# Performance work log

Measured on AMD Instinct MI355X. Metric: run time of the kernel, lower is better.

The kernel has to match this reference:

```python
import jax, jax.numpy as jnp
import numpy as np

N, E = 10000, 320000
D, H, C = 256, 8, 32   # dim, heads, head_dim (dim//num_head)
DE, DF = 64, 1024      # edge_dim, dim_ff


def setup_inputs() -> dict:
    key = jax.random.key(0)
    ks = jax.random.split(key, 32)
    s = 0.05
    n = lambda k, shp: jax.random.normal(k, shp, jnp.float32) * s
    inp = {
        "nf": jax.random.normal(ks[0], (N, D), jnp.float32),
        "ei": jax.random.randint(ks[1], (2, E), 0, N),
        "ew": jax.random.normal(ks[2], (E, DE), jnp.float32),
        # GATConv 1
        "lin1": n(ks[3], (D, H * C)), "le1": n(ks[4], (DE, H * C)),
        "asrc1": n(ks[5], (H, C)), "adst1": n(ks[6], (H, C)), "aedge1": n(ks[7], (H, C)),
        "b1": jnp.zeros((H * C,), jnp.float32),
        # GATConv 2
        "lin2": n(ks[8], (D, H * C)), "le2": n(ks[9], (DE, H * C)),
        "asrc2": n(ks[10], (H, C)), "adst2": n(ks[11], (H, C)), "aedge2": n(ks[12], (H, C)),
        "b2": jnp.zeros((H * C,), jnp.float32),
        # LayerNorms
        "g1": jnp.ones((D,), jnp.float32), "be1": jnp.zeros((D,), jnp.float32),
        "g2": jnp.ones((D,), jnp.float32), "be2": jnp.zeros((D,), jnp.float32),
        "g3": jnp.ones((D,), jnp.float32), "be3": jnp.zeros((D,), jnp.float32),
        # FFN
        "w1": n(ks[13], (D, DF)), "fb1": jnp.zeros((DF,), jnp.float32),
        "w2": n(ks[14], (DF, D)), "fb2": jnp.zeros((D,), jnp.float32),
    }
    return inp


def _ln(x, g, b, eps=1e-6):
    # annotated-transformer LayerNorm: unbiased std, eps added to std
    mu = x.mean(-1, keepdims=True)
    sd = jnp.std(x, axis=-1, ddof=1, keepdims=True)
    return g * (x - mu) / (sd + eps) + b


def _gat(x, src, dst, ea, W, We, a_s, a_d, a_e, bias):
    # PyG GATConv with edge_dim, add_self_loops=True, fill_value='mean', concat=True
    ones = jnp.ones((src.shape[0], 1), x.dtype)
    cnt = jax.ops.segment_sum(ones, dst, num_segments=N)
    loop_attr = jax.ops.segment_sum(ea, dst, num_segments=N) / jnp.maximum(cnt, 1.0)
    idx = jnp.arange(N)
    srcf = jnp.concatenate([src, idx])
    dstf = jnp.concatenate([dst, idx])
    eaf = jnp.concatenate([ea, loop_attr], axis=0)          # [E+N, DE]
    xs = (x @ W).reshape(N, H, C)                            # [N,H,C]
    ef = (eaf @ We).reshape(-1, H, C)                        # [E+N,H,C]
    a_src = (xs * a_s).sum(-1)                               # [N,H]
    a_dst = (xs * a_d).sum(-1)                               # [N,H]
    alpha = a_src[srcf] + a_dst[dstf] + (ef * a_e).sum(-1)   # [E+N,H]
    alpha = jax.nn.leaky_relu(alpha, 0.2)
    m = jax.ops.segment_max(alpha, dstf, num_segments=N)     # segment softmax
    ex = jnp.exp(alpha - m[dstf])
    den = jax.ops.segment_sum(ex, dstf, num_segments=N)
    w = ex / (den[dstf] + 1e-16)                             # [E+N,H]
    out = jax.ops.segment_sum(w[:, :, None] * xs[srcf], dstf, num_segments=N)
    return out.reshape(N, H * C) + bias


def reference(nf, ei, ew, lin1, le1, asrc1, adst1, aedge1, b1,
              lin2, le2, asrc2, adst2, aedge2, b2,
              g1, be1, g2, be2, g3, be3, w1, fb1, w2, fb2):
    src, dst = ei[0], ei[1]
    h = _gat(nf, src, dst, ew, lin1, le1, asrc1, adst1, aedge1, b1)
    nf = nf + jax.nn.leaky_relu(_ln(h, g1, be1), 0.01)
    h = _gat(nf, src, dst, ew, lin2, le2, asrc2, adst2, aedge2, b2)
    nf = nf + jax.nn.leaky_relu(_ln(h, g2, be2), 0.01)
    h = jax.nn.relu(nf @ w1 + fb1) @ w2 + fb2
    nf = nf + jax.nn.leaky_relu(_ln(h, g3, be3), 0.01)
    return nf
```

## Files before the change

kernel.cpp:

```cpp
#include <hip/hip_runtime.h>
#include <hip/hip_bf16.h>
#include <math.h>

#define D 256
#define H 8
#define C 32
#define DE 64
#define DF 1024

static inline size_t align_up(size_t x, size_t a) { return (x + a - 1) / a * a; }

typedef __attribute__((ext_vector_type(8))) short short8;
typedef __attribute__((ext_vector_type(4))) float f32x4;

__device__ inline unsigned short f2b(float x) {
    __hip_bfloat16 h = __float2bfloat16(x);
    return *reinterpret_cast<unsigned short*>(&h);
}
__device__ inline float b2f(unsigned short u) {
    return __uint_as_float(((unsigned int)u) << 16);
}

__global__ void deg_kernel(const int* __restrict__ dst, int* __restrict__ deg, int E) {
    int e = blockIdx.x * 256 + threadIdx.x;
    if (e < E) atomicAdd(&deg[dst[e]], 1);
}

__global__ void partial_sum_kernel(const int* __restrict__ deg, int* __restrict__ part, int n) {
    int i = blockIdx.x * 256 + threadIdx.x;
    int v = (i < n) ? deg[i] : 0;
    for (int o = 1; o < 64; o <<= 1) v += __shfl_xor(v, o);
    __shared__ int w4[4];
    if ((threadIdx.x & 63) == 0) w4[threadIdx.x >> 6] = v;
    __syncthreads();
    if (threadIdx.x == 0) part[blockIdx.x] = w4[0] + w4[1] + w4[2] + w4[3];
}

__global__ void scan_part_kernel(int* __restrict__ part, int nb) {
    __shared__ int buf[256];
    int t = threadIdx.x;
    buf[t] = (t < nb) ? part[t] : 0;
    __syncthreads();
    for (int s = 1; s < 256; s <<= 1) {
        int v = (t >= s) ? buf[t - s] : 0;
        __syncthreads();
        buf[t] += v;
        __syncthreads();
    }
    int excl = (t == 0) ? 0 : buf[t - 1];
    if (t < nb) part[t] = excl;
}

__global__ void scan_final_kernel(const int* __restrict__ deg, const int* __restrict__ part,
                                  int* __restrict__ off, int* __restrict__ cursor, int n) {
    int b = blockIdx.x, t = threadIdx.x, i = b * 256 + t;
    __shared__ int buf[256];
    int v = (i < n) ? deg[i] : 0;
    buf[t] = v;
    __syncthreads();
    for (int s = 1; s < 256; s <<= 1) {
        int x = (t >= s) ? buf[t - s] : 0;
        __syncthreads();
        buf[t] += x;
        __syncthreads();
    }
    int excl = part[b] + buf[t] - v;
    if (i < n) { off[i] = excl; cursor[i] = excl; }
    if (i == n - 1) off[n] = excl + v;
}

__global__ void fill_kernel(const int* __restrict__ src, const int* __restrict__ dst,
                            int* __restrict__ cursor, int* __restrict__ eid,
                            int* __restrict__ src_csr, int E) {
    int e = blockIdx.x * 256 + threadIdx.x;
    if (e < E) {
        int p = atomicAdd(&cursor[dst[e]], 1);
        eid[p] = e;
        src_csr[p] = src[e];
    }
}

__global__ void convert_bf16x8_kernel(const float* __restrict__ in, unsigned short* __restrict__ out,
                                      size_t n_valid, size_t n_total) {
    size_t i = ((size_t)blockIdx.x * 256 + threadIdx.x) * 8;
    if (i >= n_total) return;
    ushort4 o0, o1;
    if (i < n_valid) {
        float4 a = *(const float4*)&in[i];
        float4 b = *(const float4*)&in[i + 4];
        o0.x = f2b(a.x); o0.y = f2b(a.y); o0.z = f2b(a.z); o0.w = f2b(a.w);
        o1.x = f2b(b.x); o1.y = f2b(b.y); o1.z = f2b(b.z); o1.w = f2b(b.w);
    } else {
        o0.x = o0.y = o0.z = o0.w = 0;
        o1 = o0;
    }
    *(ushort4*)&out[i] = o0;
    *(ushort4*)&out[i + 4] = o1;
}

__global__ void transpose4_bf16_kernel(const float* __restrict__ lin1, const float* __restrict__ lin2,
                                       const float* __restrict__ w1, const float* __restrict__ w2,
                                       unsigned short* __restrict__ lin1T, unsigned short* __restrict__ lin2T,
                                       unsigned short* __restrict__ w1T, unsigned short* __restrict__ w2T) {
    __shared__ float tile[32][33];
    int b = blockIdx.x;
    const float* in; unsigned short* outp; int K, N, tt;
    if (b < 64)       { in = lin1; outp = lin1T; K = D;  N = D;  tt = b; }
    else if (b < 128) { in = lin2; outp = lin2T; K = D;  N = D;  tt = b - 64; }
    else if (b < 384) { in = w1;   outp = w1T;   K = D;  N = DF; tt = b - 128; }
    else              { in = w2;   outp = w2T;   K = DF; N = D;  tt = b - 384; }
    int ntn = N >> 5;
    int bn = (tt % ntn) * 32, bk = (tt / ntn) * 32;
    int tx = threadIdx.x & 31, ty = threadIdx.x >> 5;
    for (int i = ty; i < 32; i += 8)
        tile[i][tx] = in[(size_t)(bk + i) * N + bn + tx];
    __syncthreads();
    for (int i = ty; i < 32; i += 8)
        outp[(size_t)(bn + i) * K + bk + tx] = f2b(tile[tx][i]);
}

template<int BM>
__global__ __launch_bounds__(256) void mfma_gemm_kernel(
    const unsigned short* __restrict__ A, const unsigned short* __restrict__ BT,
    const float* __restrict__ bias, float* __restrict__ Cf, unsigned short* __restrict__ Cb,
    int M, int Nc, int K, int relu,
    const float* __restrict__ a_s, const float* __restrict__ a_d,
    float* __restrict__ asrcO, float* __restrict__ adstO) {
    constexpr int NR = (BM == 128) ? 4 : 2;
    constexpr int AI = BM / 32;
    __shared__ unsigned short As[BM * 64];
    __shared__ unsigned short Bs[128 * 64];
    int t = threadIdx.x;
    int lane = t & 63, w = t >> 6;
    int gm0 = blockIdx.x * BM, gn0 = blockIdx.y * 128;
    f32x4 acc[4][NR] = {};
    int srow = lane >> 3, scol = (lane & 7) * 8;
    int wm = (BM == 128) ? (w >> 1) * 64 : 0;
    int wn = (BM == 128) ? (w & 1) * 64 : w * 32;
    int fr = lane & 15, fk = (lane >> 4) * 8;

    for (int k0 = 0; k0 < K; k0 += 64) {
        __syncthreads();
#pragma unroll
        for (int i = 0; i < AI; ++i) {
            int rb = w * (8 * AI) + i * 8;
            const unsigned short* ga = A + (size_t)(gm0 + rb + srow) * K + k0 + scol;
            __builtin_amdgcn_global_load_lds(
                (const __attribute__((address_space(1))) unsigned int*)ga,
                (__attribute__((address_space(3))) unsigned int*)&As[rb * 64], 16, 0, 0);
        }
#pragma unroll
        for (int i = 0; i < 4; ++i) {
            int rb = w * 32 + i * 8;
            const unsigned short* gb = BT + (size_t)(gn0 + rb + srow) * K + k0 + scol;
            __builtin_amdgcn_global_load_lds(
                (const __attribute__((address_space(1))) unsigned int*)gb,
                (__attribute__((address_space(3))) unsigned int*)&Bs[rb * 64], 16, 0, 0);
        }
        __syncthreads();
#pragma unroll
        for (int kk = 0; kk < 64; kk += 32) {
            short8 a[4], b[NR];
#pragma unroll
            for (int m = 0; m < 4; ++m)
                a[m] = *(const short8*)&As[(wm + m * 16 + fr) * 64 + kk + fk];
#pragma unroll
            for (int n = 0; n < NR; ++n)
                b[n] = *(const short8*)&Bs[(wn + n * 16 + fr) * 64 + kk + fk];
#pragma unroll
            for (int m = 0; m < 4; ++m)
#pragma unroll
                for (int n = 0; n < NR; ++n)
                    acc[m][n] = __builtin_amdgcn_mfma_f32_16x16x32_bf16(a[m], b[n], acc[m][n], 0, 0, 0);
        }
    }
    int fcol = lane & 15, frow4 = (lane >> 4) * 4;
#pragma unroll
    for (int m = 0; m < 4; ++m) {
#pragma unroll
        for (int i = 0; i < 4; ++i) {
            int gr = gm0 + wm + m * 16 + frow4 + i;
            if (gr >= M) continue;
#pragma unroll
            for (int n = 0; n < NR; ++n) {
                int gc = gn0 + wn + n * 16 + fcol;
                float v = acc[m][n][i];
                if (bias) v += bias[gc];
                if (relu) v = fmaxf(v, 0.f);
                if (Cb) Cb[(size_t)gr * Nc + gc] = f2b(v);
                else    Cf[(size_t)gr * Nc + gc] = v;
            }
        }
    }
    if (BM == 64 && a_s) {
        int head = (gn0 >> 5) + w;
        float as0 = a_s[head * 32 + fcol], as1 = a_s[head * 32 + 16 + fcol];
        float ad0 = a_d[head * 32 + fcol], ad1 = a_d[head * 32 + 16 + fcol];
#pragma unroll
        for (int m = 0; m < 4; ++m) {
#pragma unroll
            for (int i = 0; i < 4; ++i) {
                float vs = acc[m][0][i] * as0 + acc[m][1][i] * as1;
                float vd = acc[m][0][i] * ad0 + acc[m][1][i] * ad1;
#pragma unroll
                for (int o = 1; o < 16; o <<= 1) {
                    vs += __shfl_xor(vs, o);
                    vd += __shfl_xor(vd, o);
                }
                int r = gm0 + m * 16 + frow4 + i;
                if (fcol == 0 && r < M) {
                    asrcO[r * 8 + head] = vs;
                    adstO[r * 8 + head] = vd;
                }
            }
        }
    }
}

__global__ void meT_kernel(const float* __restrict__ le1, const float* __restrict__ ae1,
                           const float* __restrict__ le2, const float* __restrict__ ae2,
                           unsigned short* __restrict__ MeT) {
    int t = threadIdx.x;
    int d = t >> 3, h = t & 7;
    float s1 = 0.f, s2 = 0.f;
    for (int c = 0; c < C; ++c) {
        s1 += le1[d * (H * C) + h * C + c] * ae1[h * C + c];
        s2 += le2[d * (H * C) + h * C + c] * ae2[h * C + c];
    }
    MeT[h * 64 + d] = f2b(s1);
    MeT[(8 + h) * 64 + d] = f2b(s2);
}

__global__ __launch_bounds__(256) void ealpha_mfma_kernel(const float* __restrict__ ew,
                                                          const unsigned short* __restrict__ MeT,
                                                          float* __restrict__ eAe, int E) {
    int t = threadIdx.x;
    int lane = t & 63, w = t >> 6;
    int e0 = blockIdx.x * 64 + w * 16;
    int r = lane & 15, g = lane >> 4;
    int er = e0 + r; if (er > E - 1) er = E - 1;
    const float* rowp = ew + (size_t)er * DE;
    float4 x0 = *(const float4*)&rowp[g * 8];
    float4 x1 = *(const float4*)&rowp[g * 8 + 4];
    float4 y0 = *(const float4*)&rowp[32 + g * 8];
    float4 y1 = *(const float4*)&rowp[32 + g * 8 + 4];
    short8 a0, a1;
    a0[0] = (short)f2b(x0.x); a0[1] = (short)f2b(x0.y); a0[2] = (short)f2b(x0.z); a0[3] = (short)f2b(x0.w);
    a0[4] = (short)f2b(x1.x); a0[5] = (short)f2b(x1.y); a0[6] = (short)f2b(x1.z); a0[7] = (short)f2b(x1.w);
    a1[0] = (short)f2b(y0.x); a1[1] = (short)f2b(y0.y); a1[2] = (short)f2b(y0.z); a1[3] = (short)f2b(y0.w);
    a1[4] = (short)f2b(y1.x); a1[5] = (short)f2b(y1.y); a1[6] = (short)f2b(y1.z); a1[7] = (short)f2b(y1.w);
    short8 b0 = *(const short8*)&MeT[r * 64 + g * 8];
    short8 b1 = *(const short8*)&MeT[r * 64 + 32 + g * 8];
    f32x4 acc = {};
    acc = __builtin_amdgcn_mfma_f32_16x16x32_bf16(a0, b0, acc, 0, 0, 0);
    acc = __builtin_amdgcn_mfma_f32_16x16x32_bf16(a1, b1, acc, 0, 0, 0);
#pragma unroll
    for (int i = 0; i < 4; ++i) {
        int ee = e0 + g * 4 + i;
        if (ee < E) eAe[(size_t)ee * 16 + r] = acc[i];
    }
}

__global__ void permute_ea_kernel(const float* __restrict__ eAe, const int* __restrict__ eid,
                                  float* __restrict__ eA1c, float* __restrict__ eA2c, int E) {
    int p = blockIdx.x * 256 + threadIdx.x;
    if (p >= E) return;
    int e = eid[p];
    const float4* src = (const float4*)&eAe[(size_t)e * 16];
    float4 v0 = src[0], v1 = src[1], v2 = src[2], v3 = src[3];
    float4* d1 = (float4*)&eA1c[(size_t)p * 8];
    float4* d2 = (float4*)&eA2c[(size_t)p * 8];
    d1[0] = v0; d1[1] = v1;
    d2[0] = v2; d2[1] = v3;
}

__global__ __launch_bounds__(256) void gat_node_kernel(
    const int* __restrict__ off, const int* __restrict__ src_csr,
    const float* __restrict__ eAc,
    const float* __restrict__ asrc, const float* __restrict__ adst,
    const unsigned short* __restrict__ xsb, const float* __restrict__ nf_in,
    const float* __restrict__ bias, const float* __restrict__ gamma,
    const float* __restrict__ beta, float* __restrict__ nf_out,
    unsigned short* __restrict__ nf_out_b, int N) {
    int lane = threadIdx.x & 63;
    int n = blockIdx.x * 4 + (threadIdx.x >> 6);
    if (n >= N) return;
    int e0 = off[n], e1 = off[n + 1], deg = e1 - e0;
    int h = lane & 7;
    int hw = lane >> 3;

    float adstn = adst[n * 8 + h];

    float acc0 = 0.f, acc1 = 0.f, acc2 = 0.f, acc3 = 0.f;
    float den0 = 0.f, easum = 0.f;
    int nb8 = (deg + 7) >> 3;

    bool act = hw < deg;
    int sp = e0 + hw;
    int s_cur = act ? src_csr[sp] : n;
    float ea_cur = act ? eAc[(size_t)sp * 8 + h] : 0.f;
    float as_cur = act ? asrc[s_cur * 8 + h] : 0.f;

    for (int it = 0; it < nb8; ++it) {
        int base = it * 8;
        bool actn = (base + 8 + hw) < deg;
        int spn = e0 + base + 8 + hw;
        int s_nx = actn ? src_csr[spn] : n;
        float ea_nx = actn ? eAc[(size_t)spn * 8 + h] : 0.f;
        float as_nx = actn ? asrc[s_nx * 8 + h] : 0.f;

        float al = as_cur + adstn + ea_cur;
        al = al > 0.f ? al : 0.2f * al;
        float ex = act ? expf(al) : 0.f;
        den0 += ex;
        easum += ea_cur;

        int lim = deg - base; if (lim > 8) lim = 8;
        if (lim == 8) {
#pragma unroll
            for (int kk = 0; kk < 8; ++kk) {
                int sl = kk * 8 + hw;
                float exk = __shfl(ex, sl);
                int sk = __shfl(s_cur, sl);
                ushort4 u = *(const ushort4*)&xsb[(size_t)sk * D + lane * 4];
                acc0 = fmaf(exk, b2f(u.x), acc0);
                acc1 = fmaf(exk, b2f(u.y), acc1);
                acc2 = fmaf(exk, b2f(u.z), acc2);
                acc3 = fmaf(exk, b2f(u.w), acc3);
            }
        } else {
            for (int kk = 0; kk < lim; ++kk) {
                int sl = kk * 8 + hw;
                float exk = __shfl(ex, sl);
                int sk = __shfl(s_cur, sl);
                ushort4 u = *(const ushort4*)&xsb[(size_t)sk * D + lane * 4];
                acc0 = fmaf(exk, b2f(u.x), acc0);
                acc1 = fmaf(exk, b2f(u.y), acc1);
                acc2 = fmaf(exk, b2f(u.z), acc2);
                acc3 = fmaf(exk, b2f(u.w), acc3);
            }
        }
        s_cur = s_nx; ea_cur = ea_nx; as_cur = as_nx; act = actn;
    }
    den0  += __shfl_xor(den0, 8);
    den0  += __shfl_xor(den0, 16);
    den0  += __shfl_xor(den0, 32);
    easum += __shfl_xor(easum, 8);
    easum += __shfl_xor(easum, 16);
    easum += __shfl_xor(easum, 32);
    float sa = easum / (float)(deg > 0 ? deg : 1);
    float als = asrc[n * 8 + h] + adstn + sa;
    als = als > 0.f ? als : 0.2f * als;
    float exSelf = expf(als);
    {
        float exs = __shfl(exSelf, hw);
        ushort4 u = *(const ushort4*)&xsb[(size_t)n * D + lane * 4];
        acc0 = fmaf(exs, b2f(u.x), acc0);
        acc1 = fmaf(exs, b2f(u.y), acc1);
        acc2 = fmaf(exs, b2f(u.z), acc2);
        acc3 = fmaf(exs, b2f(u.w), acc3);
    }
    den0 += exSelf;
    float denOwn = __shfl(den0, hw);
    float inv = 1.f / (denOwn + 1e-16f);

    int t0 = lane * 4;
    float4 bi = *(const float4*)&bias[t0];
    float o0 = acc0 * inv + bi.x;
    float o1 = acc1 * inv + bi.y;
    float o2 = acc2 * inv + bi.z;
    float o3 = acc3 * inv + bi.w;

    float s1 = o0 + o1 + o2 + o3;
    float s2 = o0 * o0 + o1 * o1 + o2 * o2 + o3 * o3;
    for (int o = 1; o < 64; o <<= 1) { s1 += __shfl_xor(s1, o); s2 += __shfl_xor(s2, o); }
    float mu = s1 / 256.f;
    float var = fmaxf((s2 - 256.f * mu * mu) / 255.f, 0.f);
    float sdv = sqrtf(var) + 1e-6f;
    float4 ga = *(const float4*)&gamma[t0];
    float4 be = *(const float4*)&beta[t0];
    float4 nin = *(const float4*)&nf_in[(size_t)n * D + t0];
    float y0 = ga.x * (o0 - mu) / sdv + be.x; y0 = y0 > 0.f ? y0 : 0.01f * y0;
    float y1 = ga.y * (o1 - mu) / sdv + be.y; y1 = y1 > 0.f ? y1 : 0.01f * y1;
    float y2 = ga.z * (o2 - mu) / sdv + be.z; y2 = y2 > 0.f ? y2 : 0.01f * y2;
    float y3 = ga.w * (o3 - mu) / sdv + be.w; y3 = y3 > 0.f ? y3 : 0.01f * y3;
    float r0 = nin.x + y0, r1 = nin.y + y1, r2 = nin.z + y2, r3 = nin.w + y3;
    float4 outv; outv.x = r0; outv.y = r1; outv.z = r2; outv.w = r3;
    *(float4*)&nf_out[(size_t)n * D + t0] = outv;
    ushort4 ob; ob.x = f2b(r0); ob.y = f2b(r1); ob.z = f2b(r2); ob.w = f2b(r3);
    *(ushort4*)&nf_out_b[(size_t)n * D + t0] = ob;
}

__global__ void ln_residual_kernel(const float* __restrict__ hin, const float* __restrict__ nf_in,
                                   const float* __restrict__ gamma, const float* __restrict__ beta,
                                   float* __restrict__ out) {
    int n = blockIdx.x, t = threadIdx.x;
    float v = hin[(size_t)n * D + t];
    float s1 = v, s2 = v * v;
    for (int o = 1; o < 64; o <<= 1) { s1 += __shfl_xor(s1, o); s2 += __shfl_xor(s2, o); }
    __shared__ float r1[4], r2[4];
    int w = t >> 6;
    if ((t & 63) == 0) { r1[w] = s1; r2[w] = s2; }
    __syncthreads();
    float tot1 = r1[0] + r1[1] + r1[2] + r1[3];
    float tot2 = r2[0] + r2[1] + r2[2] + r2[3];
    float mu = tot1 / (float)D;
    float var = fmaxf((tot2 - (float)D * mu * mu) / (float)(D - 1), 0.f);
    float sd = sqrtf(var) + 1e-6f;
    float y = gamma[t] * (v - mu) / sd + beta[t];
    y = y > 0.f ? y : 0.01f * y;
    out[(size_t)n * D + t] = nf_in[(size_t)n * D + t] + y;
}

extern "C" void kernel_launch(void* const* d_in, const int* in_sizes, int n_in,
                              void* d_out, int out_size, void* d_ws, size_t ws_size,
                              hipStream_t stream) {
    const float* nf0    = (const float*)d_in[0];
    const int*   ei     = (const int*)d_in[1];
    const float* ew     = (const float*)d_in[2];
    const float* lin1   = (const float*)d_in[3];
    const float* le1    = (const float*)d_in[4];
    const float* asrc1w = (const float*)d_in[5];
    const float* adst1w = (const float*)d_in[6];
    const float* aedge1 = (const float*)d_in[7];
    const float* b1     = (const float*)d_in[8];
    const float* lin2   = (const float*)d_in[9];
    const float* le2    = (const float*)d_in[10];
    const float* asrc2w = (const float*)d_in[11];
    const float* adst2w = (const float*)d_in[12];
    const float* aedge2 = (const float*)d_in[13];
    const float* b2     = (const float*)d_in[14];
    const float* g1     = (const float*)d_in[15];
    const float* be1    = (const float*)d_in[16];
    const float* g2     = (const float*)d_in[17];
    const float* be2    = (const float*)d_in[18];
    const float* g3     = (const float*)d_in[19];
    const float* be3    = (const float*)d_in[20];
    const float* w1     = (const float*)d_in[21];
    const float* fb1    = (const float*)d_in[22];
    const float* w2     = (const float*)d_in[23];
    const float* fb2    = (const float*)d_in[24];

    const int N = in_sizes[0] / D;
    const int E = in_sizes[1] / 2;
    const int Mpad = ((N + 127) / 128) * 128;
    const int* srcI = ei;
    const int* dstI = ei + E;

    char* ws = (char*)d_ws;
    size_t ob = 0;
    auto alloc = [&](size_t bytes) { void* p = ws + ob; ob = align_up(ob + bytes, 256); return p; };
    int*   deg     = (int*)alloc((size_t)N * 4);
    int*   csr_off = (int*)alloc((size_t)(N + 1) * 4);
    int*   cursor  = (int*)alloc((size_t)N * 4);
    int*   part    = (int*)alloc(1024);
    int*   eid     = (int*)alloc((size_t)E * 4);
    int*   src_csr = (int*)alloc((size_t)E * 4);
    unsigned short* MeT = (unsigned short*)alloc(16 * 64 * 2);
    float* asrcB   = (float*)alloc((size_t)N * H * 4);
    float* adstB   = (float*)alloc((size_t)N * H * 4);
    float* eAe     = (float*)alloc((size_t)E * 16 * 4);
    float* eA1c    = (float*)alloc((size_t)E * H * 4);
    float* eA2c    = (float*)alloc((size_t)E * H * 4);
    float* xsf     = (float*)alloc((size_t)Mpad * D * 4);
    float* nfw     = (float*)alloc((size_t)N * D * 4);
    unsigned short* xs_b  = (unsigned short*)alloc((size_t)Mpad * D * 2);
    unsigned short* Abf   = (unsigned short*)alloc((size_t)Mpad * D * 2);
    unsigned short* lin1T = (unsigned short*)alloc((size_t)D * D * 2);
    unsigned short* lin2T = (unsigned short*)alloc((size_t)D * D * 2);
    unsigned short* w1T   = (unsigned short*)alloc((size_t)DF * D * 2);
    unsigned short* w2T   = (unsigned short*)alloc((size_t)D * DF * 2);
    unsigned short* hidden = (unsigned short*)ws;
    (void)ws_size;
    float* out = (float*)d_out;

    hipMemsetAsync(deg, 0, (size_t)N * 4, stream);

    int eb = (E + 255) / 256;
    int nb = (N + 255) / 256;
    deg_kernel<<<eb, 256, 0, stream>>>(dstI, deg, E);
    partial_sum_kernel<<<nb, 256, 0, stream>>>(deg, part, N);
    scan_part_kernel<<<1, 256, 0, stream>>>(part, nb);
    scan_final_kernel<<<nb, 256, 0, stream>>>(deg, part, csr_off, cursor, N);
    fill_kernel<<<eb, 256, 0, stream>>>(srcI, dstI, cursor, eid, src_csr, E);

    meT_kernel<<<1, 512, 0, stream>>>(le1, aedge1, le2, aedge2, MeT);
    ealpha_mfma_kernel<<<(E + 63) / 64, 256, 0, stream>>>(ew, MeT, eAe, E);
    permute_ea_kernel<<<eb, 256, 0, stream>>>(eAe, eid, eA1c, eA2c, E);

    transpose4_bf16_kernel<<<640, 256, 0, stream>>>(lin1, lin2, w1, w2, lin1T, lin2T, w1T, w2T);

    const size_t nvalid = (size_t)N * D, ntot = (size_t)Mpad * D;
    int cb = (int)((ntot / 8 + 255) / 256);
    int gatb = (N + 3) / 4;

    convert_bf16x8_kernel<<<cb, 256, 0, stream>>>(nf0, Abf, nvalid, ntot);
    mfma_gemm_kernel<64><<<dim3(Mpad / 64, 2), 256, 0, stream>>>(
        Abf, lin1T, nullptr, nullptr, xs_b, N, D, D, 0, asrc1w, adst1w, asrcB, adstB);
    gat_node_kernel<<<gatb, 256, 0, stream>>>(csr_off, src_csr, eA1c, asrcB, adstB,
                                              xs_b, nf0, b1, g1, be1, nfw, Abf, N);
    mfma_gemm_kernel<64><<<dim3(Mpad / 64, 2), 256, 0, stream>>>(
        Abf, lin2T, nullptr, nullptr, xs_b, N, D, D, 0, asrc2w, adst2w, asrcB, adstB);
    gat_node_kernel<<<gatb, 256, 0, stream>>>(csr_off, src_csr, eA2c, asrcB, adstB,
                                              xs_b, nfw, b2, g2, be2, nfw, Abf, N);
    mfma_gemm_kernel<128><<<dim3(Mpad / 128, 8), 256, 0, stream>>>(
        Abf, w1T, fb1, nullptr, hidden, N, DF, D, 1, nullptr, nullptr, nullptr, nullptr);
    mfma_gemm_kernel<64><<<dim3(Mpad / 64, 2), 256, 0, stream>>>(
        hidden, w2T, fb2, xsf, nullptr, N, D, DF, 0, nullptr, nullptr, nullptr, nullptr);
    ln_residual_kernel<<<N, 256, 0, stream>>>(xsf, nfw, g3, be3, out);
}
```

Before: 263.1 us.

## Fuse FFN2 GEMM with LayerNorm residual, merge MeT into transpose, widen GAT gather

Replaces the second FFN GEMM plus the separate LayerNorm/residual kernel with a single kernel. Each block computes a full 64x256 output tile and applies bias, LayerNorm, leaky ReLU and the residual add in registers, which removes the fp32 intermediate round trip and one launch. The MeT computation moves into an extra block of the transpose kernel, saving another launch. The GAT node loop now handles 16 edges per iteration with a second prefetch stream to expose more memory parallelism, at the cost of higher register pressure and a 40KB LDS footprint in the fused GEMM, which may lower occupancy.

```diff
diff --git a/kernel.cpp b/kernel.cpp
--- a/kernel.cpp
+++ b/kernel.cpp
@@ -100,10 +100,26 @@
 
 __global__ void transpose4_bf16_kernel(const float* __restrict__ lin1, const float* __restrict__ lin2,
                                        const float* __restrict__ w1, const float* __restrict__ w2,
+                                       const float* __restrict__ le1, const float* __restrict__ ae1,
+                                       const float* __restrict__ le2, const float* __restrict__ ae2,
                                        unsigned short* __restrict__ lin1T, unsigned short* __restrict__ lin2T,
-                                       unsigned short* __restrict__ w1T, unsigned short* __restrict__ w2T) {
+                                       unsigned short* __restrict__ w1T, unsigned short* __restrict__ w2T,
+                                       unsigned short* __restrict__ MeT) {
+    int b = blockIdx.x;
+    if (b == 640) {
+        for (int t = threadIdx.x; t < 512; t += 256) {
+            int d = t >> 3, h = t & 7;
+            float s1 = 0.f, s2 = 0.f;
+            for (int c = 0; c < C; ++c) {
+                s1 += le1[d * (H * C) + h * C + c] * ae1[h * C + c];
+                s2 += le2[d * (H * C) + h * C + c] * ae2[h * C + c];
+            }
+            MeT[h * 64 + d] = f2b(s1);
+            MeT[(8 + h) * 64 + d] = f2b(s2);
+        }
+        return;
+    }
     __shared__ float tile[32][33];
-    int b = blockIdx.x;
     const float* in; unsigned short* outp; int K, N, tt;
     if (b < 64)       { in = lin1; outp = lin1T; K = D;  N = D;  tt = b; }
     else if (b < 128) { in = lin2; outp = lin2T; K = D;  N = D;  tt = b - 64; }
@@ -217,18 +233,106 @@
     }
 }
 
-__global__ void meT_kernel(const float* __restrict__ le1, const float* __restrict__ ae1,
-                           const float* __restrict__ le2, const float* __restrict__ ae2,
-                           unsigned short* __restrict__ MeT) {
-    int t = threadIdx.x;
-    int d = t >> 3, h = t & 7;
-    float s1 = 0.f, s2 = 0.f;
-    for (int c = 0; c < C; ++c) {
-        s1 += le1[d * (H * C) + h * C + c] * ae1[h * C + c];
-        s2 += le2[d * (H * C) + h * C + c] * ae2[h * C + c];
-    }
-    MeT[h * 64 + d] = f2b(s1);
-    MeT[(8 + h) * 64 + d] = f2b(s2);
+__global__ __launch_bounds__(256) void ffn2_ln_kernel(
+    const unsigned short* __restrict__ A, const unsigned short* __restrict__ BT,
+    const float* __restrict__ bias, const float* __restrict__ nf_in,
+    const float* __restrict__ gamma, const float* __restrict__ beta,
+    float* __restrict__ out, int M) {
+    __shared__ unsigned short As[64 * 64];
+    __shared__ unsigned short Bs[256 * 64];
+    __shared__ float redS1[4][64], redS2[4][64];
+    __shared__ float muS[64], invS[64];
+    int t = threadIdx.x, lane = t & 63, w = t >> 6;
+    int gm0 = blockIdx.x * 64;
+    f32x4 acc[4][4] = {};
+    int srow = lane >> 3, scol = (lane & 7) * 8;
+    int wn = w * 64;
+    int fr = lane & 15, fk = (lane >> 4) * 8;
+    for (int k0 = 0; k0 < DF; k0 += 64) {
+        __syncthreads();
+#pragma unroll
+        for (int i = 0; i < 2; ++i) {
+            int rb = w * 16 + i * 8;
+            const unsigned short* ga = A + (size_t)(gm0 + rb + srow) * DF + k0 + scol;
+            __builtin_amdgcn_global_load_lds(
+                (const __attribute__((address_space(1))) unsigned int*)ga,
+                (__attribute__((address_space(3))) unsigned int*)&As[rb * 64], 16, 0, 0);
+        }
+#pragma unroll
+        for (int i = 0; i < 8; ++i) {
+            int rb = w * 64 + i * 8;
+            const unsigned short* gb = BT + (size_t)(rb + srow) * DF + k0 + scol;
+            __builtin_amdgcn_global_load_lds(
+                (const __attribute__((address_space(1))) unsigned int*)gb,
+                (__attribute__((address_space(3))) unsigned int*)&Bs[rb * 64], 16, 0, 0);
+        }
+        __syncthreads();
+#pragma unroll
+        for (int kk = 0; kk < 64; kk += 32) {
+            short8 a[4], b[4];
+#pragma unroll
+            for (int m = 0; m < 4; ++m)
+                a[m] = *(const short8*)&As[(m * 16 + fr) * 64 + kk + fk];
+#pragma unroll
+            for (int n = 0; n < 4; ++n)
+                b[n] = *(const short8*)&Bs[(wn + n * 16 + fr) * 64 + kk + fk];
+#pragma unroll
+            for (int m = 0; m < 4; ++m)
+#pragma unroll
+                for (int n = 0; n < 4; ++n)
+                    acc[m][n] = __builtin_amdgcn_mfma_f32_16x16x32_bf16(a[m], b[n], acc[m][n], 0, 0, 0);
+        }
+    }
+    int fcol = lane & 15, frow4 = (lane >> 4) * 4;
+#pragma unroll
+    for (int m = 0; m < 4; ++m) {
+#pragma unroll
+        for (int i = 0; i < 4; ++i) {
+            float vs1 = 0.f, vs2 = 0.f;
+#pragma unroll
+            for (int n = 0; n < 4; ++n) {
+                float vv = acc[m][n][i] + bias[wn + n * 16 + fcol];
+                acc[m][n][i] = vv;
+                vs1 += vv; vs2 += vv * vv;
+            }
+#pragma unroll
+            for (int o = 1; o < 16; o <<= 1) {
+                vs1 += __shfl_xor(vs1, o);
+                vs2 += __shfl_xor(vs2, o);
+            }
+            if (fcol == 0) {
+                redS1[w][m * 16 + frow4 + i] = vs1;
+                redS2[w][m * 16 + frow4 + i] = vs2;
+            }
+        }
+    }
+    __syncthreads();
+    if (t < 64) {
+        float s1 = redS1[0][t] + redS1[1][t] + redS1[2][t] + redS1[3][t];
+        float s2 = redS2[0][t] + redS2[1][t] + redS2[2][t] + redS2[3][t];
+        float mu = s1 / 256.f;
+        float var = fmaxf((s2 - 256.f * mu * mu) / 255.f, 0.f);
+        muS[t] = mu;
+        invS[t] = 1.f / (sqrtf(var) + 1e-6f);
+    }
+    __syncthreads();
+#pragma unroll
+    for (int m = 0; m < 4; ++m) {
+#pragma unroll
+        for (int i = 0; i < 4; ++i) {
+            int r = m * 16 + frow4 + i;
+            int gr = gm0 + r;
+            if (gr >= M) continue;
+            float mu = muS[r], inv = invS[r];
+#pragma unroll
+            for (int n = 0; n < 4; ++n) {
+                int gc = wn + n * 16 + fcol;
+                float y = gamma[gc] * (acc[m][n][i] - mu) * inv + beta[gc];
+                y = y > 0.f ? y : 0.01f * y;
+                out[(size_t)gr * D + gc] = nf_in[(size_t)gr * D + gc] + y;
+            }
+        }
+    }
 }
 
 __global__ __launch_bounds__(256) void ealpha_mfma_kernel(const float* __restrict__ ew,
@@ -293,35 +397,44 @@
 
     float acc0 = 0.f, acc1 = 0.f, acc2 = 0.f, acc3 = 0.f;
     float den0 = 0.f, easum = 0.f;
-    int nb8 = (deg + 7) >> 3;
-
-    bool act = hw < deg;
-    int sp = e0 + hw;
-    int s_cur = act ? src_csr[sp] : n;
-    float ea_cur = act ? eAc[(size_t)sp * 8 + h] : 0.f;
-    float as_cur = act ? asrc[s_cur * 8 + h] : 0.f;
-
-    for (int it = 0; it < nb8; ++it) {
-        int base = it * 8;
-        bool actn = (base + 8 + hw) < deg;
-        int spn = e0 + base + 8 + hw;
-        int s_nx = actn ? src_csr[spn] : n;
-        float ea_nx = actn ? eAc[(size_t)spn * 8 + h] : 0.f;
-        float as_nx = actn ? asrc[s_nx * 8 + h] : 0.f;
-
-        float al = as_cur + adstn + ea_cur;
-        al = al > 0.f ? al : 0.2f * al;
-        float ex = act ? expf(al) : 0.f;
-        den0 += ex;
-        easum += ea_cur;
-
-        int lim = deg - base; if (lim > 8) lim = 8;
-        if (lim == 8) {
-#pragma unroll
-            for (int kk = 0; kk < 8; ++kk) {
-                int sl = kk * 8 + hw;
-                float exk = __shfl(ex, sl);
-                int sk = __shfl(s_cur, sl);
+    int nb16 = (deg + 15) >> 4;
+
+    bool actA = hw < deg, actB = (8 + hw) < deg;
+    int spA = e0 + hw, spB = e0 + 8 + hw;
+    int sA = actA ? src_csr[spA] : n;
+    int sB = actB ? src_csr[spB] : n;
+    float eaA = actA ? eAc[(size_t)spA * 8 + h] : 0.f;
+    float eaB = actB ? eAc[(size_t)spB * 8 + h] : 0.f;
+    float asA = actA ? asrc[sA * 8 + h] : 0.f;
+    float asB = actB ? asrc[sB * 8 + h] : 0.f;
+
+    for (int it = 0; it < nb16; ++it) {
+        int base = it * 16;
+        bool actAn = (base + 16 + hw) < deg, actBn = (base + 24 + hw) < deg;
+        int spAn = e0 + base + 16 + hw, spBn = e0 + base + 24 + hw;
+        int sAn = actAn ? src_csr[spAn] : n;
+        int sBn = actBn ? src_csr[spBn] : n;
+        float eaAn = actAn ? eAc[(size_t)spAn * 8 + h] : 0.f;
+        float eaBn = actBn ? eAc[(size_t)spBn * 8 + h] : 0.f;
+        float asAn = actAn ? asrc[sAn * 8 + h] : 0.f;
+        float asBn = actBn ? asrc[sBn * 8 + h] : 0.f;
+
+        float alA = asA + adstn + eaA;
+        alA = alA > 0.f ? alA : 0.2f * alA;
+        float exA = actA ? expf(alA) : 0.f;
+        float alB = asB + adstn + eaB;
+        alB = alB > 0.f ? alB : 0.2f * alB;
+        float exB = actB ? expf(alB) : 0.f;
+        den0 += exA + exB;
+        easum += eaA + eaB;
+
+        int lim = deg - base; if (lim > 16) lim = 16;
+        if (lim == 16) {
+#pragma unroll
+            for (int kk = 0; kk < 16; ++kk) {
+                int sl = (kk & 7) * 8 + hw;
+                float exk = (kk < 8) ? __shfl(exA, sl) : __shfl(exB, sl);
+                int sk = (kk < 8) ? __shfl(sA, sl) : __shfl(sB, sl);
                 ushort4 u = *(const ushort4*)&xsb[(size_t)sk * D + lane * 4];
                 acc0 = fmaf(exk, b2f(u.x), acc0);
                 acc1 = fmaf(exk, b2f(u.y), acc1);
@@ -330,9 +443,9 @@
             }
         } else {
             for (int kk = 0; kk < lim; ++kk) {
-                int sl = kk * 8 + hw;
-                float exk = __shfl(ex, sl);
-                int sk = __shfl(s_cur, sl);
+                int sl = (kk & 7) * 8 + hw;
+                float exk = (kk < 8) ? __shfl(exA, sl) : __shfl(exB, sl);
+                int sk = (kk < 8) ? __shfl(sA, sl) : __shfl(sB, sl);
                 ushort4 u = *(const ushort4*)&xsb[(size_t)sk * D + lane * 4];
                 acc0 = fmaf(exk, b2f(u.x), acc0);
                 acc1 = fmaf(exk, b2f(u.y), acc1);
@@ -340,7 +453,8 @@
                 acc3 = fmaf(exk, b2f(u.w), acc3);
             }
         }
-        s_cur = s_nx; ea_cur = ea_nx; as_cur = as_nx; act = actn;
+        sA = sAn; sB = sBn; eaA = eaAn; eaB = eaBn; asA = asAn; asB = asBn;
+        actA = actAn; actB = actBn;
     }
     den0  += __shfl_xor(den0, 8);
     den0  += __shfl_xor(den0, 16);
@@ -389,27 +503,6 @@
     *(float4*)&nf_out[(size_t)n * D + t0] = outv;
     ushort4 ob; ob.x = f2b(r0); ob.y = f2b(r1); ob.z = f2b(r2); ob.w = f2b(r3);
     *(ushort4*)&nf_out_b[(size_t)n * D + t0] = ob;
-}
-
-__global__ void ln_residual_kernel(const float* __restrict__ hin, const float* __restrict__ nf_in,
-                                   const float* __restrict__ gamma, const float* __restrict__ beta,
-                                   float* __restrict__ out) {
-    int n = blockIdx.x, t = threadIdx.x;
-    float v = hin[(size_t)n * D + t];
-    float s1 = v, s2 = v * v;
-    for (int o = 1; o < 64; o <<= 1) { s1 += __shfl_xor(s1, o); s2 += __shfl_xor(s2, o); }
-    __shared__ float r1[4], r2[4];
-    int w = t >> 6;
-    if ((t & 63) == 0) { r1[w] = s1; r2[w] = s2; }
-    __syncthreads();
-    float tot1 = r1[0] + r1[1] + r1[2] + r1[3];
-    float tot2 = r2[0] + r2[1] + r2[2] + r2[3];
-    float mu = tot1 / (float)D;
-    float var = fmaxf((tot2 - (float)D * mu * mu) / (float)(D - 1), 0.f);
-    float sd = sqrtf(var) + 1e-6f;
-    float y = gamma[t] * (v - mu) / sd + beta[t];
-    y = y > 0.f ? y : 0.01f * y;
-    out[(size_t)n * D + t] = nf_in[(size_t)n * D + t] + y;
 }
 
 extern "C" void kernel_launch(void* const* d_in, const int* in_sizes, int n_in,
@@ -462,7 +555,6 @@
     float* eAe     = (float*)alloc((size_t)E * 16 * 4);
     float* eA1c    = (float*)alloc((size_t)E * H * 4);
     float* eA2c    = (float*)alloc((size_t)E * H * 4);
-    float* xsf     = (float*)alloc((size_t)Mpad * D * 4);
     float* nfw     = (float*)alloc((size_t)N * D * 4);
     unsigned short* xs_b  = (unsigned short*)alloc((size_t)Mpad * D * 2);
     unsigned short* Abf   = (unsigned short*)alloc((size_t)Mpad * D * 2);
@@ -484,11 +576,10 @@
     scan_final_kernel<<<nb, 256, 0, stream>>>(deg, part, csr_off, cursor, N);
     fill_kernel<<<eb, 256, 0, stream>>>(srcI, dstI, cursor, eid, src_csr, E);
 
-    meT_kernel<<<1, 512, 0, stream>>>(le1, aedge1, le2, aedge2, MeT);
+    transpose4_bf16_kernel<<<641, 256, 0, stream>>>(lin1, lin2, w1, w2, le1, aedge1, le2, aedge2,
+                                                    lin1T, lin2T, w1T, w2T, MeT);
     ealpha_mfma_kernel<<<(E + 63) / 64, 256, 0, stream>>>(ew, MeT, eAe, E);
     permute_ea_kernel<<<eb, 256, 0, stream>>>(eAe, eid, eA1c, eA2c, E);
-
-    transpose4_bf16_kernel<<<640, 256, 0, stream>>>(lin1, lin2, w1, w2, lin1T, lin2T, w1T, w2T);
 
     const size_t nvalid = (size_t)N * D, ntot = (size_t)Mpad * D;
     int cb = (int)((ntot / 8 + 255) / 256);
@@ -504,8 +595,6 @@
     gat_node_kernel<<<gatb, 256, 0, stream>>>(csr_off, src_csr, eA2c, asrcB, adstB,
                                               xs_b, nfw, b2, g2, be2, nfw, Abf, N);
     mfma_gemm_kernel<128><<<dim3(Mpad / 128, 8), 256, 0, stream>>>(
-        Abf, w1T, fb1, nullptr, hidden, N, DF, D, 1, nullptr, nullptr, nullptr, nullptr);
-    mfma_gemm_kernel<64><<<dim3(Mpad / 64, 2), 256, 0, stream>>>(
-        hidden, w2T, fb2, xsf, nullptr, N, D, DF, 0, nullptr, nullptr, nullptr, nullptr);
-    ln_residual_kernel<<<N, 256, 0, stream>>>(xsf, nfw, g3, be3, out);
-}
+        Abf, w1T, fb1, nullptr, hidden, Mpad, DF, D, 1, nullptr, nullptr, nullptr, nullptr);
+    ffn2_ln_kernel<<<(N + 63) / 64, 256, 0, stream>>>(hidden, w2T, fb2, nfw, g3, be3, out, N);
+}
```

Result: no change. 259.4 us (-1.4%).
